# Kernel optimization log

Hardware: AMD Instinct MI355X
Metric: run time of the kernel (lower is better)

Reference implementation:

```python
import jax, jax.numpy as jnp
import numpy as np

W = 5  # fine window size


def setup_inputs() -> dict:
    key = jax.random.key(0)
    ks = jax.random.split(key, 10)
    bs, d_f, h_f, w_f = 4, 64, 240, 320
    d_c, L_c = 256, 4800  # coarse feats flattened over 60x80 grid
    N = 16384  # number of matched fine points
    feat_f0 = jax.random.normal(ks[0], (bs, d_f, h_f, w_f), jnp.float32)
    feat_f1 = jax.random.normal(ks[1], (bs, d_f, h_f, w_f), jnp.float32)
    feat_c0 = jax.random.normal(ks[2], (bs, L_c, d_c), jnp.float32)
    feat_c1 = jax.random.normal(ks[3], (bs, L_c, d_c), jnp.float32)
    b_ids = jax.random.randint(ks[4], (N,), 0, bs, jnp.int32)
    # window centers clamped to the valid interior: [W//2, dim - W//2)
    center_y = jax.random.randint(ks[5], (N,), 0, h_f - W + 1, jnp.int32) + W // 2
    center_x = jax.random.randint(ks[6], (N,), 0, w_f - W + 1, jnp.int32) + W // 2
    ci_ids = jax.random.randint(ks[7], (N,), 0, L_c, jnp.int32)
    # kaiming_normal_(mode='fan_out'): std = sqrt(2 / fan_out)
    Wd = jax.random.normal(ks[8], (d_c, d_f), jnp.float32) * np.sqrt(2.0 / d_f)
    bd = jnp.zeros((d_f,), jnp.float32)
    Wm = jax.random.normal(ks[9], (2 * d_f, d_f), jnp.float32) * np.sqrt(2.0 / d_f)
    bm = jnp.zeros((d_f,), jnp.float32)
    return {"feat_f0": feat_f0, "feat_f1": feat_f1, "feat_c0": feat_c0,
            "feat_c1": feat_c1, "Wd": Wd, "bd": bd, "Wm": Wm, "bm": bm,
            "b_ids": b_ids, "center_y": center_y, "center_x": center_x,
            "ci_ids": ci_ids}


def reference(feat_f0, feat_f1, feat_c0, feat_c1, Wd, bd, Wm, bm,
              b_ids, center_y, center_x, ci_ids):
    # torch.arange(-W//2+1, W//2+1) == [-(W//2), ..., W//2] for odd W
    off = jnp.arange(-(W // 2), W // 2 + 1, dtype=jnp.int32)
    gy = jnp.repeat(off, W)   # [W*W] row-major y offsets
    gx = jnp.tile(off, W)     # [W*W] row-major x offsets
    y_ids = center_y[:, None] + gy[None, :]   # [N, WW]
    x_ids = center_x[:, None] + gx[None, :]   # [N, WW]
    # gather WxW windows: feat_f[b, :, y, x] -> [N, WW, d_f]
    f0u = feat_f0[b_ids[:, None], :, y_ids, x_ids]
    f1u = feat_f1[b_ids[:, None], :, y_ids, x_ids]
    # gather coarse features at the matched coarse cells -> [N, d_c]
    c0 = feat_c0[b_ids, ci_ids]
    c1 = feat_c1[b_ids, ci_ids]
    # down_proj over the stacked (0/1) coarse feats -> [2N, d_f]
    c_win = jnp.concatenate([c0, c1], axis=0) @ Wd + bd
    f_cat = jnp.concatenate([f0u, f1u], axis=0)           # [2N, WW, d_f]
    WW = f_cat.shape[1]
    c_rep = jnp.broadcast_to(c_win[:, None, :], (c_win.shape[0], WW, c_win.shape[1]))
    merged = jnp.concatenate([f_cat, c_rep], axis=-1) @ Wm + bm  # [2N, WW, d_f]
    f0_out, f1_out = jnp.split(merged, 2, axis=0)
    return (f0_out, f1_out)
```

## Files before the change

kernel.cpp:

```cpp
#include <hip/hip_runtime.h>

#define WIN 5
#define WW 25
#define DF 64
#define DC 256
#define HF 240
#define WF 320
#define LC 4800
#define NQ 16384
#define CH_STRIDE ((size_t)HF * WF)
#define BS_STRIDE_F ((size_t)DF * CH_STRIDE)
#define FPAD 68
#define FB 72

#define WS_WFUSED 0
#define WS_BFUSED (DC * DF)
#define WS_CPART  (DC * DF + 256)
#define WS_WMT    (WS_CPART + 2 * NQ * DF)
#define WS_FT     (WS_WMT + 2048)
#define MAPSZ_US  ((size_t)4 * CH_STRIDE * DF)
#define WS_NEEDED_BYTES ((size_t)WS_FT * 4 + 2 * MAPSZ_US * 2)

typedef __attribute__((ext_vector_type(8))) short bf16x8;
typedef __attribute__((ext_vector_type(4))) float f32x4;

__device__ __forceinline__ unsigned short f2bf(float x) {
    unsigned int u = __float_as_uint(x);
    u += 0x7FFFu + ((u >> 16) & 1u);
    return (unsigned short)(u >> 16);
}

__global__ __launch_bounds__(64) void k0_fuse_weights(
    const float* __restrict__ Wd, const float* __restrict__ bd,
    const float* __restrict__ Wm, const float* __restrict__ bm,
    float* __restrict__ ws)
{
    const int r = blockIdx.x;
    const int j = threadIdx.x;
    if (r < DC) {
        float acc = 0.f;
        #pragma unroll 8
        for (int i = 0; i < DF; ++i)
            acc += Wd[r * DF + i] * Wm[(DF + i) * DF + j];
        ws[WS_WFUSED + r * DF + j] = acc;
    } else if (r == DC) {
        float acc = bm[j];
        #pragma unroll 8
        for (int i = 0; i < DF; ++i)
            acc += bd[i] * Wm[(DF + i) * DF + j];
        ws[WS_BFUSED + j] = acc;
    } else {
        unsigned short* __restrict__ wmT = (unsigned short*)(ws + WS_WMT);
        #pragma unroll 8
        for (int i = 0; i < DF; ++i)
            wmT[j * DF + i] = f2bf(Wm[i * DF + j]);
    }
}

#define K1_ROWS 16
__global__ __launch_bounds__(256) void k1_cpart(
    const float* __restrict__ c0, const float* __restrict__ c1,
    const int* __restrict__ b_ids, const int* __restrict__ ci,
    float* __restrict__ ws)
{
    const float* __restrict__ wfused = ws + WS_WFUSED;
    const float* __restrict__ bfused = ws + WS_BFUSED;
    float* __restrict__ cpart = ws + WS_CPART;

    const int t  = threadIdx.x;
    const int j  = t & 63;
    const int kc = t >> 6;

    float wf[64];
    #pragma unroll
    for (int k = 0; k < 64; ++k)
        wf[k] = wfused[(kc * 64 + k) * DF + j];

    __shared__ float c_sh[DC];
    __shared__ float red[256];

    for (int ri = 0; ri < K1_ROWS; ++ri) {
        const int row = blockIdx.x * K1_ROWS + ri;
        const int s = row >> 14;
        const int n = row & (NQ - 1);
        const float* __restrict__ fc = s ? c1 : c0;
        const int b  = b_ids[n];
        const int cc = ci[n];

        c_sh[t] = fc[((size_t)b * LC + cc) * DC + t];
        __syncthreads();

        float acc = 0.f;
        #pragma unroll
        for (int k4 = 0; k4 < 16; ++k4) {
            float4 cv = *(const float4*)&c_sh[kc * 64 + k4 * 4];
            acc += cv.x * wf[k4 * 4 + 0] + cv.y * wf[k4 * 4 + 1] +
                   cv.z * wf[k4 * 4 + 2] + cv.w * wf[k4 * 4 + 3];
        }
        red[t] = acc;
        __syncthreads();

        if (t < 64) {
            cpart[(size_t)row * DF + t] =
                red[t] + red[t + 64] + red[t + 128] + red[t + 192] + bfused[t];
        }
    }
}

__global__ __launch_bounds__(256) void kt_transpose(
    const float* __restrict__ f0, const float* __restrict__ f1,
    float* __restrict__ ws)
{
    const int t = threadIdx.x;
    const float* __restrict__ src = blockIdx.z ? f1 : f0;
    unsigned short* __restrict__ fT =
        (unsigned short*)(ws + WS_FT) + (size_t)blockIdx.z * MAPSZ_US;
    const int b  = blockIdx.y;
    const int p0 = blockIdx.x * 64;

    __shared__ float tile[64][65];

    const float* __restrict__ sb = src + (size_t)b * BS_STRIDE_F;
    const int g  = t >> 4;
    const int x4 = t & 15;
    #pragma unroll
    for (int q = 0; q < 4; ++q) {
        const int c = g + q * 16;
        const float4 v = *(const float4*)&sb[(size_t)c * CH_STRIDE + p0 + x4 * 4];
        tile[c][x4 * 4 + 0] = v.x; tile[c][x4 * 4 + 1] = v.y;
        tile[c][x4 * 4 + 2] = v.z; tile[c][x4 * 4 + 3] = v.w;
    }
    __syncthreads();
    unsigned short* __restrict__ ob = fT + ((size_t)b * CH_STRIDE + p0) * DF;
    #pragma unroll
    for (int q = 0; q < 4; ++q) {
        const int p  = g + q * 16;
        const int cc = x4 * 4;
        ushort4 h;
        h.x = f2bf(tile[cc + 0][p]); h.y = f2bf(tile[cc + 1][p]);
        h.z = f2bf(tile[cc + 2][p]); h.w = f2bf(tile[cc + 3][p]);
        *(ushort4*)&ob[(size_t)p * DF + cc] = h;
    }
}

__global__ __launch_bounds__(256) void k2_mfma(
    const int* __restrict__ b_ids, const int* __restrict__ cy,
    const int* __restrict__ cx,
    const float* __restrict__ ws, float* __restrict__ out)
{
    const float* __restrict__ cpart = ws + WS_CPART;
    const unsigned short* __restrict__ wmT = (const unsigned short*)(ws + WS_WMT);

    const int t    = threadIdx.x;
    const int lane = t & 63;
    const int wave = t >> 6;

    __shared__ unsigned short wmT_sh[DF * FB];
    __shared__ unsigned short f_sh[4 * WW * FB];

    #pragma unroll
    for (int q = 0; q < 2; ++q) {
        const int idx = t + q * 256;
        const int j   = idx >> 3;
        const int sg  = idx & 7;
        *(uint4*)&wmT_sh[j * FB + sg * 8] = *(const uint4*)&wmT[j * DF + sg * 8];
    }

    const int gw = blockIdx.x * 4 + wave;
    const int s  = gw >> 14;
    const int n  = gw & (NQ - 1);
    const unsigned short* __restrict__ fTm =
        (const unsigned short*)(ws + WS_FT) + (size_t)s * MAPSZ_US;
    const int b = b_ids[n];
    const int Y = cy[n];
    const int X = cx[n];
    const int base = ((b * HF + (Y - 2)) * WF + (X - 2)) * DF;

    unsigned short* fw = f_sh + wave * WW * FB;
    #pragma unroll
    for (int r = 0; r < 4; ++r) {
        const int e = lane + r * 64;
        if (e < 200) {
            const int w  = e >> 3;
            const int sg = e & 7;
            const int wy = (w * 13) >> 6;
            const int wx = w - wy * 5;
            *(uint4*)&fw[w * FB + sg * 8] =
                *(const uint4*)&fTm[base + (wy * WF + wx) * DF + sg * 8];
        }
    }
    __syncthreads();

    const int row16 = lane & 15;
    const int kb    = lane >> 4;
    const int r1row = (row16 < 9) ? (16 + row16) : 24;

    f32x4 acc[2][4];
    #pragma unroll
    for (int m = 0; m < 2; ++m)
        #pragma unroll
        for (int nn = 0; nn < 4; ++nn)
            acc[m][nn] = (f32x4){0.f, 0.f, 0.f, 0.f};

    #pragma unroll
    for (int ks = 0; ks < 2; ++ks) {
        const int k0 = ks * 32 + kb * 8;
        const bf16x8 a0 = *(const bf16x8*)&fw[row16 * FB + k0];
        const bf16x8 a1 = *(const bf16x8*)&fw[r1row * FB + k0];
        #pragma unroll
        for (int nn = 0; nn < 4; ++nn) {
            const bf16x8 bfrag = *(const bf16x8*)&wmT_sh[(nn * 16 + row16) * FB + k0];
            acc[0][nn] = __builtin_amdgcn_mfma_f32_16x16x32_bf16(a0, bfrag, acc[0][nn], 0, 0, 0);
            acc[1][nn] = __builtin_amdgcn_mfma_f32_16x16x32_bf16(a1, bfrag, acc[1][nn], 0, 0, 0);
        }
    }

    const float* __restrict__ cprow = cpart + (size_t)gw * DF;
    float* __restrict__ ob = out + (size_t)gw * (WW * DF);
    #pragma unroll
    for (int nn = 0; nn < 4; ++nn) {
        const float cp = cprow[nn * 16 + row16];
        #pragma unroll
        for (int m = 0; m < 2; ++m) {
            #pragma unroll
            for (int r = 0; r < 4; ++r) {
                const int w = m * 16 + kb * 4 + r;
                if (w < WW)
                    ob[w * DF + nn * 16 + row16] = acc[m][nn][r] + cp;
            }
        }
    }
}

__global__ __launch_bounds__(256) void k2_main(
    const float* __restrict__ f0, const float* __restrict__ f1,
    const float* __restrict__ Wm,
    const int* __restrict__ b_ids, const int* __restrict__ cy,
    const int* __restrict__ cx,
    const float* __restrict__ ws, float* __restrict__ out)
{
    const float* __restrict__ cpart = ws + WS_CPART;

    const int t    = threadIdx.x;
    const int lane = t & 63;
    const int wave = t >> 6;

    __shared__ float wm_sh[DF * DF];
    __shared__ float f_sh[4 * WW * FPAD];

    {
        const float4* src = (const float4*)Wm;
        float4* dst = (float4*)wm_sh;
        #pragma unroll
        for (int q = 0; q < 4; ++q)
            dst[t + q * 256] = src[t + q * 256];
    }

    const int gw = blockIdx.x * 4 + wave;
    const int s  = gw >> 14;
    const int n  = gw & (NQ - 1);
    const float* __restrict__ ff = s ? f1 : f0;
    const int b = b_ids[n];
    const int Y = cy[n];
    const int X = cx[n];

    float* fw = f_sh + wave * WW * FPAD;
    const float* fwin = ff + (size_t)b * BS_STRIDE_F + (size_t)(Y - 2) * WF + (X - 2);
    #pragma unroll
    for (int r = 0; r < 25; ++r) {
        const int e = lane + r * 64;
        const int i = e / 25;
        const int w = e - i * 25;
        const int wy = w / 5;
        const int wx = w - wy * 5;
        fw[w * FPAD + i] = fwin[(size_t)i * CH_STRIDE + wy * WF + wx];
    }
    __syncthreads();

    const int j0 = (lane & 15) * 4;
    const int w0 = lane >> 4;

    const float4 cp = *(const float4*)&cpart[(size_t)gw * DF + j0];
    float4 acc[7];
    #pragma unroll
    for (int u = 0; u < 7; ++u) acc[u] = cp;

    #pragma unroll 4
    for (int i = 0; i < DF; i += 4) {
        const float4 m0 = *(const float4*)&wm_sh[(i + 0) * DF + j0];
        const float4 m1 = *(const float4*)&wm_sh[(i + 1) * DF + j0];
        const float4 m2 = *(const float4*)&wm_sh[(i + 2) * DF + j0];
        const float4 m3 = *(const float4*)&wm_sh[(i + 3) * DF + j0];
        #pragma unroll
        for (int u = 0; u < 7; ++u) {
            const int w = w0 + 4 * u;
            if (w < WW) {
                const float4 fv = *(const float4*)&fw[w * FPAD + i];
                acc[u].x += fv.x * m0.x + fv.y * m1.x + fv.z * m2.x + fv.w * m3.x;
                acc[u].y += fv.x * m0.y + fv.y * m1.y + fv.z * m2.y + fv.w * m3.y;
                acc[u].z += fv.x * m0.z + fv.y * m1.z + fv.z * m2.z + fv.w * m3.z;
                acc[u].w += fv.x * m0.w + fv.y * m1.w + fv.z * m2.w + fv.w * m3.w;
            }
        }
    }

    float* ob = out + (size_t)gw * (WW * DF);
    #pragma unroll
    for (int u = 0; u < 7; ++u) {
        const int w = w0 + 4 * u;
        if (w < WW)
            *(float4*)&ob[w * DF + j0] = acc[u];
    }
}

extern "C" void kernel_launch(void* const* d_in, const int* in_sizes, int n_in,
                              void* d_out, int out_size, void* d_ws, size_t ws_size,
                              hipStream_t stream) {
    const float* f0 = (const float*)d_in[0];
    const float* f1 = (const float*)d_in[1];
    const float* c0 = (const float*)d_in[2];
    const float* c1 = (const float*)d_in[3];
    const float* Wd = (const float*)d_in[4];
    const float* bd = (const float*)d_in[5];
    const float* Wm = (const float*)d_in[6];
    const float* bm = (const float*)d_in[7];
    const int* b_ids = (const int*)d_in[8];
    const int* cyv   = (const int*)d_in[9];
    const int* cxv   = (const int*)d_in[10];
    const int* civ   = (const int*)d_in[11];
    float* out = (float*)d_out;
    float* ws  = (float*)d_ws;

    const bool big_ws = (ws_size >= WS_NEEDED_BYTES);

    if (big_ws) {
        kt_transpose<<<dim3(CH_STRIDE / 64, 4, 2), dim3(256), 0, stream>>>(f0, f1, ws);
    }
    k0_fuse_weights<<<dim3(DC + 2), dim3(64), 0, stream>>>(Wd, bd, Wm, bm, ws);
    k1_cpart<<<dim3(2 * NQ / K1_ROWS), dim3(256), 0, stream>>>(c0, c1, b_ids, civ, ws);
    if (big_ws) {
        k2_mfma<<<dim3(2 * NQ / 4), dim3(256), 0, stream>>>(
            b_ids, cyv, cxv, ws, out);
    } else {
        k2_main<<<dim3(2 * NQ / 4), dim3(256), 0, stream>>>(
            f0, f1, Wm, b_ids, cyv, cxv, ws, out);
    }
}
```

Baseline: 461.1 us.

## Load MFMA fragments directly from global memory and use nontemporal loads and stores

Removes the LDS staging of the weight matrix and the gathered window features in the MFMA kernel. Each lane now loads its bf16x8 A and B fragments straight from global memory into registers, which also drops the __syncthreads. The transpose kernel's input reads and the output stores switch to nontemporal builtins to limit cache pollution on streaming traffic. The trade-off is that the weight fragments are re-read per wave from global or L2 instead of shared memory, and direct fragment loads may coalesce less well.

```diff
diff --git a/kernel.cpp b/kernel.cpp
--- a/kernel.cpp
+++ b/kernel.cpp
@@ -11,7 +11,6 @@
 #define CH_STRIDE ((size_t)HF * WF)
 #define BS_STRIDE_F ((size_t)DF * CH_STRIDE)
 #define FPAD 68
-#define FB 72
 
 #define WS_WFUSED 0
 #define WS_BFUSED (DC * DF)
@@ -126,9 +125,10 @@
     #pragma unroll
     for (int q = 0; q < 4; ++q) {
         const int c = g + q * 16;
-        const float4 v = *(const float4*)&sb[(size_t)c * CH_STRIDE + p0 + x4 * 4];
-        tile[c][x4 * 4 + 0] = v.x; tile[c][x4 * 4 + 1] = v.y;
-        tile[c][x4 * 4 + 2] = v.z; tile[c][x4 * 4 + 3] = v.w;
+        const f32x4 v = __builtin_nontemporal_load(
+            (const f32x4*)&sb[(size_t)c * CH_STRIDE + p0 + x4 * 4]);
+        tile[c][x4 * 4 + 0] = v[0]; tile[c][x4 * 4 + 1] = v[1];
+        tile[c][x4 * 4 + 2] = v[2]; tile[c][x4 * 4 + 3] = v[3];
     }
     __syncthreads();
     unsigned short* __restrict__ ob = fT + ((size_t)b * CH_STRIDE + p0) * DF;
@@ -155,16 +155,16 @@
     const int lane = t & 63;
     const int wave = t >> 6;
 
-    __shared__ unsigned short wmT_sh[DF * FB];
-    __shared__ unsigned short f_sh[4 * WW * FB];
-
-    #pragma unroll
-    for (int q = 0; q < 2; ++q) {
-        const int idx = t + q * 256;
-        const int j   = idx >> 3;
-        const int sg  = idx & 7;
-        *(uint4*)&wmT_sh[j * FB + sg * 8] = *(const uint4*)&wmT[j * DF + sg * 8];
-    }
+    const int row16 = lane & 15;
+    const int kb    = lane >> 4;
+
+    bf16x8 bfr[2][4];
+    #pragma unroll
+    for (int ks = 0; ks < 2; ++ks)
+        #pragma unroll
+        for (int nn = 0; nn < 4; ++nn)
+            bfr[ks][nn] = *(const bf16x8*)
+                &wmT[(nn * 16 + row16) * DF + ks * 32 + kb * 8];
 
     const int gw = blockIdx.x * 4 + wave;
     const int s  = gw >> 14;
@@ -176,24 +176,19 @@
     const int X = cx[n];
     const int base = ((b * HF + (Y - 2)) * WF + (X - 2)) * DF;
 
-    unsigned short* fw = f_sh + wave * WW * FB;
-    #pragma unroll
-    for (int r = 0; r < 4; ++r) {
-        const int e = lane + r * 64;
-        if (e < 200) {
-            const int w  = e >> 3;
-            const int sg = e & 7;
-            const int wy = (w * 13) >> 6;
-            const int wx = w - wy * 5;
-            *(uint4*)&fw[w * FB + sg * 8] =
-                *(const uint4*)&fTm[base + (wy * WF + wx) * DF + sg * 8];
-        }
-    }
-    __syncthreads();
-
-    const int row16 = lane & 15;
-    const int kb    = lane >> 4;
-    const int r1row = (row16 < 9) ? (16 + row16) : 24;
+    const int w0  = row16;
+    const int w1  = (row16 < 9) ? (16 + row16) : 24;
+    const int wy0 = (w0 * 13) >> 6;
+    const int wy1 = (w1 * 13) >> 6;
+    const unsigned short* __restrict__ fq0 =
+        fTm + base + (wy0 * WF + (w0 - wy0 * 5)) * DF + kb * 8;
+    const unsigned short* __restrict__ fq1 =
+        fTm + base + (wy1 * WF + (w1 - wy1 * 5)) * DF + kb * 8;
+
+    const bf16x8 a00 = *(const bf16x8*)(fq0);
+    const bf16x8 a01 = *(const bf16x8*)(fq0 + 32);
+    const bf16x8 a10 = *(const bf16x8*)(fq1);
+    const bf16x8 a11 = *(const bf16x8*)(fq1 + 32);
 
     f32x4 acc[2][4];
     #pragma unroll
@@ -203,16 +198,11 @@
             acc[m][nn] = (f32x4){0.f, 0.f, 0.f, 0.f};
 
     #pragma unroll
-    for (int ks = 0; ks < 2; ++ks) {
-        const int k0 = ks * 32 + kb * 8;
-        const bf16x8 a0 = *(const bf16x8*)&fw[row16 * FB + k0];
-        const bf16x8 a1 = *(const bf16x8*)&fw[r1row * FB + k0];
-        #pragma unroll
-        for (int nn = 0; nn < 4; ++nn) {
-            const bf16x8 bfrag = *(const bf16x8*)&wmT_sh[(nn * 16 + row16) * FB + k0];
-            acc[0][nn] = __builtin_amdgcn_mfma_f32_16x16x32_bf16(a0, bfrag, acc[0][nn], 0, 0, 0);
-            acc[1][nn] = __builtin_amdgcn_mfma_f32_16x16x32_bf16(a1, bfrag, acc[1][nn], 0, 0, 0);
-        }
+    for (int nn = 0; nn < 4; ++nn) {
+        acc[0][nn] = __builtin_amdgcn_mfma_f32_16x16x32_bf16(a00, bfr[0][nn], acc[0][nn], 0, 0, 0);
+        acc[1][nn] = __builtin_amdgcn_mfma_f32_16x16x32_bf16(a10, bfr[0][nn], acc[1][nn], 0, 0, 0);
+        acc[0][nn] = __builtin_amdgcn_mfma_f32_16x16x32_bf16(a01, bfr[1][nn], acc[0][nn], 0, 0, 0);
+        acc[1][nn] = __builtin_amdgcn_mfma_f32_16x16x32_bf16(a11, bfr[1][nn], acc[1][nn], 0, 0, 0);
     }
 
     const float* __restrict__ cprow = cpart + (size_t)gw * DF;
@@ -226,7 +216,8 @@
             for (int r = 0; r < 4; ++r) {
                 const int w = m * 16 + kb * 4 + r;
                 if (w < WW)
-                    ob[w * DF + nn * 16 + row16] = acc[m][nn][r] + cp;
+                    __builtin_nontemporal_store(
+                        acc[m][nn][r] + cp, &ob[w * DF + nn * 16 + row16]);
             }
         }
     }
```

Result: faster. 438.1 us (-5.0%).
